# Kernel optimization log

Hardware: AMD Instinct MI355X
Metric: run time of the kernel (lower is better)

Reference implementation:

```python
import jax, jax.numpy as jnp
from jax import lax
import numpy as np

B, L, F = 4, 1024, 32
DM, NL, DS, DC, EX, NH = 256, 4, 16, 4, 2, 4
DI = EX * DM            # 512 inner channels
DTR = (DM + 15) // 16   # dt_rank = 16


def setup_inputs() -> dict:
    key = jax.random.key(0)
    ks = jax.random.split(key, 12)
    s = 0.02
    rn = lambda k, shape: jax.random.normal(k, shape, jnp.float32) * s
    return dict(
        x=jax.random.normal(ks[0], (B, L, F), jnp.float32),
        proj_w=rn(ks[1], (DM, F)), proj_b=jnp.zeros((DM,), jnp.float32),
        inproj_w=rn(ks[2], (NL, 2 * DI, DM)),
        conv_w=rn(ks[3], (NL, DI, DC)), conv_b=jnp.zeros((NL, DI), jnp.float32),
        xproj_w=rn(ks[4], (NL, DTR + 2 * DS, DI)),
        dtproj_w=rn(ks[5], (NL, DI, DTR)), dtproj_b=rn(ks[6], (NL, DI)),
        A_log=jnp.tile(jnp.log(jnp.arange(1, DS + 1, dtype=jnp.float32))[None, None, :], (NL, DI, 1)),
        Dp=jnp.ones((NL, DI), jnp.float32),
        outproj_w=rn(ks[7], (NL, DM, DI)),
        ln_g=jnp.ones((NL, DM), jnp.float32), ln_b=jnp.zeros((NL, DM), jnp.float32),
        head_w1=rn(ks[8], (DM, DM)), head_b1=jnp.zeros((DM,), jnp.float32),
        head_w2=rn(ks[9], (NH, DM)), head_b2=jnp.zeros((NH,), jnp.float32),
    )


def _layernorm(x, g, b, eps=1e-5):
    mu = x.mean(axis=-1, keepdims=True)
    var = ((x - mu) ** 2).mean(axis=-1, keepdims=True)
    return (x - mu) * lax.rsqrt(var + eps) * g + b


def _mamba(x, inw, cw, cb, xpw, dtw, dtb, A_log, Dp, outw):
    b, l, _ = x.shape
    xz = x @ inw.T                       # (b,l,2*DI)
    u, z = xz[..., :DI], xz[..., DI:]
    # causal depthwise conv1d, kernel DC
    up = jnp.pad(u, ((0, 0), (DC - 1, 0), (0, 0)))
    uc = sum(up[:, k:k + l, :] * cw[:, k] for k in range(DC)) + cb
    uc = jax.nn.silu(uc)
    dbc = uc @ xpw.T                     # (b,l,DTR+2*DS)
    dt, Bc, Cc = dbc[..., :DTR], dbc[..., DTR:DTR + DS], dbc[..., DTR + DS:]
    delta = jax.nn.softplus(dt @ dtw.T + dtb)   # (b,l,DI)
    A = -jnp.exp(A_log)                  # (DI,DS)

    def step(h, inp):
        d_t, B_t, C_t, u_t = inp         # (b,DI),(b,DS),(b,DS),(b,DI)
        h = jnp.exp(d_t[..., None] * A) * h + (d_t * u_t)[..., None] * B_t[:, None, :]
        return h, jnp.einsum('bdn,bn->bd', h, C_t)

    h0 = jnp.zeros((b, DI, DS), x.dtype)
    xs = tuple(jnp.swapaxes(a, 0, 1) for a in (delta, Bc, Cc, uc))
    _, ys = lax.scan(step, h0, xs)       # ys: (l,b,DI)
    y = jnp.swapaxes(ys, 0, 1) + uc * Dp
    return (y * jax.nn.silu(z)) @ outw.T


def reference(x, proj_w, proj_b, inproj_w, conv_w, conv_b, xproj_w, dtproj_w, dtproj_b,
              A_log, Dp, outproj_w, ln_g, ln_b, head_w1, head_b1, head_w2, head_b2):
    h = x @ proj_w.T + proj_b
    for i in range(NL):
        blk = _mamba(h, inproj_w[i], conv_w[i], conv_b[i], xproj_w[i],
                     dtproj_w[i], dtproj_b[i], A_log[i], Dp[i], outproj_w[i])
        h = h + _layernorm(blk, ln_g[i], ln_b[i])
    p = h.mean(axis=1)                   # (b,DM) pool over time
    hid = jax.nn.relu(p @ head_w1.T + head_b1)
    return hid @ head_w2.T + head_b2     # (b,NH)
```

## Files before the change

### kernel.cpp

```cpp
#include <hip/hip_runtime.h>
#include <hip/hip_fp16.h>
#include <math.h>

#define LTOT 1024
#define BB   4
#define F_IN 32
#define DM   256
#define DI   512
#define DS   16
#define DTRN 16
#define NXP  48
#define NLAY 4
#define NH   4
#define NC   16
#define CLEN 64
#define ROWS (BB*LTOT)

typedef _Float16 half8 __attribute__((ext_vector_type(8)));
typedef float f32x16 __attribute__((ext_vector_type(16)));

__device__ __forceinline__ float siluf_(float x) { return x / (1.0f + expf(-x)); }
__device__ __forceinline__ float softplusf_(float x) {
    if (x > 20.f) return x;
    if (x < -20.f) return expf(x);
    return log1pf(expf(x));
}

__device__ __forceinline__ void split16(float x, unsigned short& hi, unsigned short& lo) {
    __half h = __float2half(x);
    hi = *(unsigned short*)&h;
    float r = x - __half2float(h);
    __half l = __float2half(r);
    lo = *(unsigned short*)&l;
}

__global__ __launch_bounds__(256) void k_proj(const float* __restrict__ x,
                                              const float* __restrict__ pw,
                                              const float* __restrict__ pb,
                                              float* __restrict__ h) {
    __shared__ float wl[DM][33];
    __shared__ float xl[16][32];
    int t = threadIdx.x;
    int r0 = blockIdx.x * 16;
    for (int i = t; i < DM * 32 / 4; i += 256) {
        float4 v = ((const float4*)pw)[i];
        int c = i / 8, k = (i % 8) * 4;
        wl[c][k] = v.x; wl[c][k + 1] = v.y; wl[c][k + 2] = v.z; wl[c][k + 3] = v.w;
    }
    for (int i = t; i < 16 * 32 / 4; i += 256) {
        float4 v = ((const float4*)(x + (size_t)r0 * F_IN))[i];
        int r = i / 8, k = (i % 8) * 4;
        xl[r][k] = v.x; xl[r][k + 1] = v.y; xl[r][k + 2] = v.z; xl[r][k + 3] = v.w;
    }
    __syncthreads();
    int c = t;
    float bias = pb[c];
    float acc[16];
#pragma unroll
    for (int r = 0; r < 16; ++r) acc[r] = bias;
    for (int k = 0; k < 32; ++k) {
        float w = wl[c][k];
#pragma unroll
        for (int r = 0; r < 16; ++r) acc[r] = fmaf(xl[r][k], w, acc[r]);
    }
#pragma unroll
    for (int r = 0; r < 16; ++r) h[(size_t)(r0 + r) * DM + c] = acc[r];
}

__global__ __launch_bounds__(256) void k_gemm_xz(const float* __restrict__ A,
                                                 const float* __restrict__ Bw,
                                                 float* __restrict__ C) {
    __shared__ unsigned short Ah[128][40], Al[128][40], Bh[128][40], Bl[128][40];
    int t = threadIdx.x;
    int bx = blockIdx.x & 7;
    int by = blockIdx.x >> 3;
    int srow = t & 127, sh = t >> 7;
    const float* Ap = A + (size_t)(by * 128 + srow) * DM + sh * 16;
    const float* Bp = Bw + (size_t)(bx * 128 + srow) * DM + sh * 16;
    float4 pa[4], pb[4];
#pragma unroll
    for (int j = 0; j < 4; ++j) {
        pa[j] = *(const float4*)(Ap + j * 4);
        pb[j] = *(const float4*)(Bp + j * 4);
    }
    int lane = t & 63, wid = t >> 6;
    int fr = lane & 31, fg = lane >> 5;
    f32x16 acc[4] = {};
    for (int k0 = 0; k0 < DM; k0 += 32) {
        __syncthreads();
#pragma unroll
        for (int j = 0; j < 4; ++j) {
            ushort4 h4, l4;
            split16(pa[j].x, h4.x, l4.x); split16(pa[j].y, h4.y, l4.y);
            split16(pa[j].z, h4.z, l4.z); split16(pa[j].w, h4.w, l4.w);
            *(ushort4*)&Ah[srow][sh * 16 + j * 4] = h4;
            *(ushort4*)&Al[srow][sh * 16 + j * 4] = l4;
            split16(pb[j].x, h4.x, l4.x); split16(pb[j].y, h4.y, l4.y);
            split16(pb[j].z, h4.z, l4.z); split16(pb[j].w, h4.w, l4.w);
            *(ushort4*)&Bh[srow][sh * 16 + j * 4] = h4;
            *(ushort4*)&Bl[srow][sh * 16 + j * 4] = l4;
        }
        __syncthreads();
        if (k0 + 32 < DM) {
#pragma unroll
            for (int j = 0; j < 4; ++j) {
                pa[j] = *(const float4*)(Ap + k0 + 32 + j * 4);
                pb[j] = *(const float4*)(Bp + k0 + 32 + j * 4);
            }
        }
#pragma unroll
        for (int s = 0; s < 2; ++s) {
            int ko = s * 16 + fg * 8;
            half8 ah = *(const half8*)&Ah[wid * 32 + fr][ko];
            half8 al = *(const half8*)&Al[wid * 32 + fr][ko];
#pragma unroll
            for (int fc = 0; fc < 4; ++fc) {
                half8 bh = *(const half8*)&Bh[fc * 32 + fr][ko];
                half8 bl = *(const half8*)&Bl[fc * 32 + fr][ko];
                acc[fc] = __builtin_amdgcn_mfma_f32_32x32x16_f16(ah, bh, acc[fc], 0, 0, 0);
                acc[fc] = __builtin_amdgcn_mfma_f32_32x32x16_f16(ah, bl, acc[fc], 0, 0, 0);
                acc[fc] = __builtin_amdgcn_mfma_f32_32x32x16_f16(al, bh, acc[fc], 0, 0, 0);
            }
        }
    }
    float* Cp = C + (size_t)(by * 128 + wid * 32) * 1024 + bx * 128;
#pragma unroll
    for (int fc = 0; fc < 4; ++fc) {
#pragma unroll
        for (int reg = 0; reg < 16; ++reg) {
            int row = (reg & 3) + 8 * (reg >> 2) + 4 * fg;
            Cp[(size_t)row * 1024 + fc * 32 + fr] = acc[fc][reg];
        }
    }
}

__global__ __launch_bounds__(256) void k_conv(const float* __restrict__ xz,
                                              const float* __restrict__ cw,
                                              const float* __restrict__ cb,
                                              float* __restrict__ uc) {
    int gid = blockIdx.x * 256 + threadIdx.x;
    if (gid >= ROWS * (DI / 4)) return;
    int r = gid / (DI / 4);
    int d = (gid % (DI / 4)) * 4;
    int tt = r & (LTOT - 1);
    float4 acc = make_float4(cb[d], cb[d + 1], cb[d + 2], cb[d + 3]);
#pragma unroll
    for (int k = 0; k < 4; ++k) {
        int ts = tt - 3 + k;
        if (ts < 0) continue;
        float4 u = *(const float4*)(xz + (size_t)(r - 3 + k) * 1024 + d);
        acc.x = fmaf(u.x, cw[(d + 0) * 4 + k], acc.x);
        acc.y = fmaf(u.y, cw[(d + 1) * 4 + k], acc.y);
        acc.z = fmaf(u.z, cw[(d + 2) * 4 + k], acc.z);
        acc.w = fmaf(u.w, cw[(d + 3) * 4 + k], acc.w);
    }
    acc.x = siluf_(acc.x); acc.y = siluf_(acc.y); acc.z = siluf_(acc.z); acc.w = siluf_(acc.w);
    *(float4*)(uc + (size_t)r * DI + d) = acc;
}

__global__ __launch_bounds__(256) void k_dbcp(const float* __restrict__ uc,
                                              const float* __restrict__ xpw,
                                              float* __restrict__ xz) {
    __shared__ float us[32][132];
    __shared__ float wsd[48][132];
    int t = threadIdx.x;
    int kp = blockIdx.x & 3;
    int r0 = (blockIdx.x >> 2) * 32;
    int k0 = kp * 128;
    float4* us4 = (float4*)us;
    float4* ws4 = (float4*)wsd;
#pragma unroll
    for (int j = 0; j < 4; ++j) {
        int i = t + j * 256;
        int r = i >> 5, kq = i & 31;
        us4[r * 33 + kq] = *(const float4*)(uc + (size_t)(r0 + r) * DI + k0 + kq * 4);
    }
#pragma unroll
    for (int j = 0; j < 6; ++j) {
        int i = t + j * 256;
        int r = i >> 5, kq = i & 31;
        ws4[r * 33 + kq] = *(const float4*)(xpw + (size_t)r * DI + k0 + kq * 4);
    }
    __syncthreads();
    int tx = t & 15, ty = t >> 4;
    const float4* ua = us4 + (ty * 2) * 33;
    const float4* ub = ua + 33;
    const float4* w0p = ws4 + (tx * 3) * 33;
    const float4* w1p = w0p + 33;
    const float4* w2p = w0p + 66;
    float acc[2][3] = {};
#pragma unroll 4
    for (int kq = 0; kq < 32; ++kq) {
        float4 u0 = ua[kq], u1 = ub[kq];
        float4 w0 = w0p[kq], w1 = w1p[kq], w2 = w2p[kq];
        acc[0][0] = fmaf(u0.x, w0.x, acc[0][0]); acc[0][0] = fmaf(u0.y, w0.y, acc[0][0]);
        acc[0][0] = fmaf(u0.z, w0.z, acc[0][0]); acc[0][0] = fmaf(u0.w, w0.w, acc[0][0]);
        acc[0][1] = fmaf(u0.x, w1.x, acc[0][1]); acc[0][1] = fmaf(u0.y, w1.y, acc[0][1]);
        acc[0][1] = fmaf(u0.z, w1.z, acc[0][1]); acc[0][1] = fmaf(u0.w, w1.w, acc[0][1]);
        acc[0][2] = fmaf(u0.x, w2.x, acc[0][2]); acc[0][2] = fmaf(u0.y, w2.y, acc[0][2]);
        acc[0][2] = fmaf(u0.z, w2.z, acc[0][2]); acc[0][2] = fmaf(u0.w, w2.w, acc[0][2]);
        acc[1][0] = fmaf(u1.x, w0.x, acc[1][0]); acc[1][0] = fmaf(u1.y, w0.y, acc[1][0]);
        acc[1][0] = fmaf(u1.z, w0.z, acc[1][0]); acc[1][0] = fmaf(u1.w, w0.w, acc[1][0]);
        acc[1][1] = fmaf(u1.x, w1.x, acc[1][1]); acc[1][1] = fmaf(u1.y, w1.y, acc[1][1]);
        acc[1][1] = fmaf(u1.z, w1.z, acc[1][1]); acc[1][1] = fmaf(u1.w, w1.w, acc[1][1]);
        acc[1][2] = fmaf(u1.x, w2.x, acc[1][2]); acc[1][2] = fmaf(u1.y, w2.y, acc[1][2]);
        acc[1][2] = fmaf(u1.z, w2.z, acc[1][2]); acc[1][2] = fmaf(u1.w, w2.w, acc[1][2]);
    }
    float* outp = xz + (size_t)(r0 + ty * 2) * 1024 + kp * 48 + tx * 3;
    outp[0] = acc[0][0]; outp[1] = acc[0][1]; outp[2] = acc[0][2];
    outp[1024] = acc[1][0]; outp[1025] = acc[1][1]; outp[1026] = acc[1][2];
}

__global__ __launch_bounds__(256) void k_dbcr(const float* __restrict__ xzp,
                                              const float* __restrict__ dtw,
                                              const float* __restrict__ dtb,
                                              float* __restrict__ delta,
                                              float* __restrict__ BC) {
    __shared__ float dbl[16][NXP];
    int t = threadIdx.x;
    int r0 = blockIdx.x * 16;
    {
        int r = t >> 4, c3 = (t & 15) * 3;
        const float* pp = xzp + (size_t)(r0 + r) * 1024 + c3;
#pragma unroll
        for (int j = 0; j < 3; ++j) {
            float s = pp[j] + pp[48 + j] + pp[96 + j] + pp[144 + j];
            dbl[r][c3 + j] = s;
            int cj = c3 + j;
            if (cj >= 16) BC[(size_t)(r0 + r) * 32 + (cj - 16)] = s;
        }
    }
    __syncthreads();
    {
        int c0 = t * 2;
        float wd0[16], wd1[16];
        const float4* q0 = (const float4*)(dtw + (size_t)c0 * 16);
        const float4* q1 = (const float4*)(dtw + (size_t)(c0 + 1) * 16);
#pragma unroll
        for (int j = 0; j < 4; ++j) { *(float4*)&wd0[j * 4] = q0[j]; *(float4*)&wd1[j * 4] = q1[j]; }
        float bb0 = dtb[c0], bb1 = dtb[c0 + 1];
        for (int r = 0; r < 16; ++r) {
            float s0 = bb0, s1 = bb1;
#pragma unroll
            for (int k = 0; k < 16; ++k) {
                float dv = dbl[r][k];
                s0 = fmaf(dv, wd0[k], s0);
                s1 = fmaf(dv, wd1[k], s1);
            }
            *(float2*)(delta + (size_t)(r0 + r) * DI + c0) =
                make_float2(softplusf_(s0), softplusf_(s1));
        }
    }
}

__global__ __launch_bounds__(256) void k_scanA(const float* __restrict__ delta,
                                               const float* __restrict__ uc,
                                               const float* __restrict__ BC,
                                               const float* __restrict__ A_log,
                                               float* __restrict__ P,
                                               float* __restrict__ hL) {
    __shared__ float2 du2[CLEN][16];
    __shared__ float  Bl[CLEN][16];
    int bid = blockIdx.x;
    int c = bid & 15, dblk = (bid >> 4) & 31, b = bid >> 9;
    int d0 = dblk * 16, t0 = c * CLEN;
    int t = threadIdx.x;
    {
        int row = t >> 2, hf = (t & 3) * 4;
        size_t rbase = (size_t)(b * LTOT + t0 + row);
        float4 dv = *(const float4*)(delta + rbase * DI + d0 + hf);
        float4 uv = *(const float4*)(uc + rbase * DI + d0 + hf);
        float4* dst = (float4*)&du2[row][hf];
        dst[0] = make_float4(dv.x, uv.x, dv.y, uv.y);
        dst[1] = make_float4(dv.z, uv.z, dv.w, uv.w);
        *(float4*)&Bl[row][hf] = *(const float4*)(BC + rbase * 32 + hf);
    }
    __syncthreads();
    int n = t & 15, dn = t >> 4;
    float Ac = -expf(A_log[(size_t)(d0 + dn) * DS + n]);
    float h = 0.f, Pp = 1.f;
#pragma unroll 8
    for (int k = 0; k < CLEN; ++k) {
        float2 du = du2[k][dn];
        float Bv = Bl[k][n];
        float a = expf(du.x * Ac);
        Pp *= a;
        h = fmaf(a, h, du.x * du.y * Bv);
    }
    size_t idx = ((size_t)(b * NC + c)) * (DI * DS) + (size_t)d0 * DS + t;
    P[idx] = Pp;
    hL[idx] = h;
}

__global__ __launch_bounds__(256) void k_scanC(const float* __restrict__ delta,
                                               const float* __restrict__ uc,
                                               const float* __restrict__ BC,
                                               const float* __restrict__ A_log,
                                               const float* __restrict__ P,
                                               const float* __restrict__ hL,
                                               const float* __restrict__ Dp,
                                               float* __restrict__ xz) {
    __shared__ float2 du2[CLEN][16];
    __shared__ float2 bc2[CLEN][16];
    __shared__ float  ytmp[16][16][20];
    int bid = blockIdx.x;
    int c = bid & 15, dblk = (bid >> 4) & 31, b = bid >> 9;
    int d0 = dblk * 16, t0 = c * CLEN;
    int t = threadIdx.x;
    {
        int row = t >> 2, hf = (t & 3) * 4;
        size_t rbase = (size_t)(b * LTOT + t0 + row);
        float4 dv = *(const float4*)(delta + rbase * DI + d0 + hf);
        float4 uv = *(const float4*)(uc + rbase * DI + d0 + hf);
        float4* dst = (float4*)&du2[row][hf];
        dst[0] = make_float4(dv.x, uv.x, dv.y, uv.y);
        dst[1] = make_float4(dv.z, uv.z, dv.w, uv.w);
        float4 bv = *(const float4*)(BC + rbase * 32 + hf);
        float4 cv = *(const float4*)(BC + rbase * 32 + 16 + hf);
        float4* bdst = (float4*)&bc2[row][hf];
        bdst[0] = make_float4(bv.x, cv.x, bv.y, cv.y);
        bdst[1] = make_float4(bv.z, cv.z, bv.w, cv.w);
    }
    __syncthreads();
    int n = t & 15, dn = t >> 4;
    float Ac = -expf(A_log[(size_t)(d0 + dn) * DS + n]);
    float Hin = 0.f;
    for (int cc = 0; cc < c; ++cc) {
        size_t idx = ((size_t)(b * NC + cc)) * (DI * DS) + (size_t)d0 * DS + t;
        Hin = fmaf(P[idx], Hin, hL[idx]);
    }
    float h = Hin;
    int rdn = t & 15, rk = t >> 4;
    float DpV = Dp[d0 + rdn];
    for (int s = 0; s < CLEN / 16; ++s) {
#pragma unroll
        for (int kk = 0; kk < 16; ++kk) {
            int k = s * 16 + kk;
            float2 du = du2[k][dn];
            float2 bc = bc2[k][n];
            float a = expf(du.x * Ac);
            h = fmaf(a, h, du.x * du.y * bc.x);
            ytmp[kk][dn][n] = h * bc.y;
        }
        __syncthreads();
        {
            const float* rowp = &ytmp[rk][rdn][0];
            float4 v0 = *(const float4*)(rowp + 0);
            float4 v1 = *(const float4*)(rowp + 4);
            float4 v2 = *(const float4*)(rowp + 8);
            float4 v3 = *(const float4*)(rowp + 12);
            float y = ((v0.x + v0.y) + (v0.z + v0.w)) + ((v1.x + v1.y) + (v1.z + v1.w))
                    + ((v2.x + v2.y) + (v2.z + v2.w)) + ((v3.x + v3.y) + (v3.z + v3.w));
            float uu = du2[s * 16 + rk][rdn].y;
            size_t rb2 = (size_t)(b * LTOT + t0 + s * 16 + rk);
            float z = xz[rb2 * 1024 + 512 + d0 + rdn];
            xz[rb2 * 1024 + d0 + rdn] = fmaf(uu, DpV, y) * siluf_(z);
        }
        __syncthreads();
    }
}

__global__ __launch_bounds__(256) void k_gemm_out(const float* __restrict__ xz,
                                                  const float* __restrict__ outw,
                                                  float* __restrict__ p01,
                                                  float* __restrict__ p23) {
    __shared__ unsigned short Ah[128][40], Al[128][40], Bh[128][40], Bl[128][40];
    int t = threadIdx.x;
    int bx = blockIdx.x & 1;
    int by = (blockIdx.x >> 1) & 31;
    int kp = blockIdx.x >> 6;
    int srow = t & 127, sh = t >> 7;
    const float* Ap = xz + (size_t)(by * 128 + srow) * 1024 + kp * 128 + sh * 16;
    const float* Bp = outw + (size_t)(bx * 128 + srow) * DI + kp * 128 + sh * 16;
    float4 pa[4], pb[4];
#pragma unroll
    for (int j = 0; j < 4; ++j) {
        pa[j] = *(const float4*)(Ap + j * 4);
        pb[j] = *(const float4*)(Bp + j * 4);
    }
    int lane = t & 63, wid = t >> 6;
    int fr = lane & 31, fg = lane >> 5;
    f32x16 acc[4] = {};
    for (int k0 = 0; k0 < 128; k0 += 32) {
        __syncthreads();
#pragma unroll
        for (int j = 0; j < 4; ++j) {
            ushort4 h4, l4;
            split16(pa[j].x, h4.x, l4.x); split16(pa[j].y, h4.y, l4.y);
            split16(pa[j].z, h4.z, l4.z); split16(pa[j].w, h4.w, l4.w);
            *(ushort4*)&Ah[srow][sh * 16 + j * 4] = h4;
            *(ushort4*)&Al[srow][sh * 16 + j * 4] = l4;
            split16(pb[j].x, h4.x, l4.x); split16(pb[j].y, h4.y, l4.y);
            split16(pb[j].z, h4.z, l4.z); split16(pb[j].w, h4.w, l4.w);
            *(ushort4*)&Bh[srow][sh * 16 + j * 4] = h4;
            *(ushort4*)&Bl[srow][sh * 16 + j * 4] = l4;
        }
        __syncthreads();
        if (k0 + 32 < 128) {
#pragma unroll
            for (int j = 0; j < 4; ++j) {
                pa[j] = *(const float4*)(Ap + k0 + 32 + j * 4);
                pb[j] = *(const float4*)(Bp + k0 + 32 + j * 4);
            }
        }
#pragma unroll
        for (int s = 0; s < 2; ++s) {
            int ko = s * 16 + fg * 8;
            half8 ah = *(const half8*)&Ah[wid * 32 + fr][ko];
            half8 al = *(const half8*)&Al[wid * 32 + fr][ko];
#pragma unroll
            for (int fc = 0; fc < 4; ++fc) {
                half8 bh = *(const half8*)&Bh[fc * 32 + fr][ko];
                half8 bl = *(const half8*)&Bl[fc * 32 + fr][ko];
                acc[fc] = __builtin_amdgcn_mfma_f32_32x32x16_f16(ah, bh, acc[fc], 0, 0, 0);
                acc[fc] = __builtin_amdgcn_mfma_f32_32x32x16_f16(ah, bl, acc[fc], 0, 0, 0);
                acc[fc] = __builtin_amdgcn_mfma_f32_32x32x16_f16(al, bh, acc[fc], 0, 0, 0);
            }
        }
    }
    float* pbase = (kp < 2 ? p01 : p23) + (size_t)(kp & 1) * (ROWS * DM);
    float* Cp = pbase + (size_t)(by * 128 + wid * 32) * DM + bx * 128;
#pragma unroll
    for (int fc = 0; fc < 4; ++fc) {
#pragma unroll
        for (int reg = 0; reg < 16; ++reg) {
            int row = (reg & 3) + 8 * (reg >> 2) + 4 * fg;
            Cp[(size_t)row * DM + fc * 32 + fr] = acc[fc][reg];
        }
    }
}

__global__ __launch_bounds__(256) void k_ln_res(const float* __restrict__ p01,
                                                const float* __restrict__ p23,
                                                const float* __restrict__ g,
                                                const float* __restrict__ bb,
                                                float* __restrict__ h) {
    __shared__ float scratch[4];
    int r = blockIdx.x, t = threadIdx.x;
    size_t idx = (size_t)r * DM + t;
    float v = p01[idx] + p01[idx + (size_t)ROWS * DM] + p23[idx] + p23[idx + (size_t)ROWS * DM];
    float s = v;
#pragma unroll
    for (int m = 32; m >= 1; m >>= 1) s += __shfl_xor(s, m, 64);
    if ((t & 63) == 0) scratch[t >> 6] = s;
    __syncthreads();
    float mu = (scratch[0] + scratch[1] + scratch[2] + scratch[3]) * (1.f / DM);
    __syncthreads();
    float d = v - mu;
    float s2 = d * d;
#pragma unroll
    for (int m = 32; m >= 1; m >>= 1) s2 += __shfl_xor(s2, m, 64);
    if ((t & 63) == 0) scratch[t >> 6] = s2;
    __syncthreads();
    float var = (scratch[0] + scratch[1] + scratch[2] + scratch[3]) * (1.f / DM);
    float rstd = 1.f / sqrtf(var + 1e-5f);
    h[idx] += d * rstd * g[t] + bb[t];
}

__global__ __launch_bounds__(256) void k_meanp(const float* __restrict__ h,
                                               float* __restrict__ part) {
    int bid = blockIdx.x;
    int b = bid >> 3, g = bid & 7;
    int t = threadIdx.x;
    float s = 0.f;
    for (int k = 0; k < 128; ++k)
        s += h[(size_t)(b * LTOT + g * 128 + k) * DM + t];
    part[(size_t)bid * DM + t] = s;
}

__global__ __launch_bounds__(256) void k_head(const float* __restrict__ part,
                                              const float* __restrict__ w1,
                                              const float* __restrict__ b1,
                                              const float* __restrict__ w2,
                                              const float* __restrict__ b2,
                                              float* __restrict__ out) {
    __shared__ float pl[DM], hl[DM];
    int b = blockIdx.x, t = threadIdx.x;
    float s = 0.f;
    for (int g = 0; g < 8; ++g) s += part[(size_t)(b * 8 + g) * DM + t];
    pl[t] = s * (1.f / LTOT);
    __syncthreads();
    float a = b1[t];
    for (int k = 0; k < DM; ++k) a = fmaf(pl[k], w1[(size_t)t * DM + k], a);
    hl[t] = fmaxf(a, 0.f);
    __syncthreads();
    if (t < NH) {
        float o = b2[t];
        for (int k = 0; k < DM; ++k) o = fmaf(hl[k], w2[(size_t)t * DM + k], o);
        out[b * NH + t] = o;
    }
}

extern "C" void kernel_launch(void* const* d_in, const int* in_sizes, int n_in,
                              void* d_out, int out_size, void* d_ws, size_t ws_size,
                              hipStream_t stream) {
    const float* x        = (const float*)d_in[0];
    const float* proj_w   = (const float*)d_in[1];
    const float* proj_b   = (const float*)d_in[2];
    const float* inproj_w = (const float*)d_in[3];
    const float* conv_w   = (const float*)d_in[4];
    const float* conv_b   = (const float*)d_in[5];
    const float* xproj_w  = (const float*)d_in[6];
    const float* dtproj_w = (const float*)d_in[7];
    const float* dtproj_b = (const float*)d_in[8];
    const float* A_log    = (const float*)d_in[9];
    const float* Dp       = (const float*)d_in[10];
    const float* outproj_w= (const float*)d_in[11];
    const float* ln_g     = (const float*)d_in[12];
    const float* ln_b     = (const float*)d_in[13];
    const float* head_w1  = (const float*)d_in[14];
    const float* head_b1  = (const float*)d_in[15];
    const float* head_w2  = (const float*)d_in[16];
    const float* head_b2  = (const float*)d_in[17];

    float* ws    = (float*)d_ws;
    float* h     = ws;
    float* xz    = h + 1048576;
    float* uc    = xz + 4194304;
    float* delta = uc + 2097152;
    float* BC    = delta + 2097152;
    float* Pbuf  = BC + 131072;
    float* hLbuf = Pbuf + 524288;
    float* part  = hLbuf + 524288;

    k_proj<<<ROWS / 16, 256, 0, stream>>>(x, proj_w, proj_b, h);

    for (int i = 0; i < NLAY; ++i) {
        const float* inw  = inproj_w + (size_t)i * (2 * DI) * DM;
        const float* cwi  = conv_w + (size_t)i * DI * 4;
        const float* cbi  = conv_b + (size_t)i * DI;
        const float* xpw  = xproj_w + (size_t)i * NXP * DI;
        const float* dtw  = dtproj_w + (size_t)i * DI * DTRN;
        const float* dtb  = dtproj_b + (size_t)i * DI;
        const float* Ali  = A_log + (size_t)i * DI * DS;
        const float* Dpi  = Dp + (size_t)i * DI;
        const float* outw = outproj_w + (size_t)i * DM * DI;
        const float* gi   = ln_g + (size_t)i * DM;
        const float* bi   = ln_b + (size_t)i * DM;

        k_gemm_xz<<<256, 256, 0, stream>>>(h, inw, xz);
        k_conv<<<ROWS * (DI / 4) / 256, 256, 0, stream>>>(xz, cwi, cbi, uc);
        k_dbcp<<<512, 256, 0, stream>>>(uc, xpw, xz);
        k_dbcr<<<ROWS / 16, 256, 0, stream>>>(xz, dtw, dtb, delta, BC);
        k_scanA<<<BB * 32 * NC, 256, 0, stream>>>(delta, uc, BC, Ali, Pbuf, hLbuf);
        k_scanC<<<BB * 32 * NC, 256, 0, stream>>>(delta, uc, BC, Ali, Pbuf, hLbuf, Dpi, xz);
        k_gemm_out<<<256, 256, 0, stream>>>(xz, outw, delta, uc);
        k_ln_res<<<ROWS, 256, 0, stream>>>(delta, uc, gi, bi, h);
    }

    k_meanp<<<32, 256, 0, stream>>>(h, part);
    k_head<<<BB, 256, 0, stream>>>(part, head_w1, head_b1, head_w2, head_b2, (float*)d_out);
}
```

Baseline: 533.5 us.

## Pre-split GEMM operands into fp16 hi/lo in producers and shrink GEMM tiles

Weights for in_proj and out_proj are split into fp16 hi/lo halves once per call by a new kernel. Activations are split in the producing kernels (proj, layernorm-residual, scanC) and written as separate hi/lo buffers, so the GEMMs load ready-made halves instead of converting inside the main loop. The GEMM tile shrinks from 128x128 to 64x128, doubling the grid to 512 blocks for better occupancy. The cost is extra global writes for the hi/lo buffers, more workspace, and one added kernel launch.

```diff
diff --git a/kernel.cpp b/kernel.cpp
--- a/kernel.cpp
+++ b/kernel.cpp
@@ -18,6 +18,7 @@
 
 typedef _Float16 half8 __attribute__((ext_vector_type(8)));
 typedef float f32x16 __attribute__((ext_vector_type(16)));
+typedef unsigned short us8 __attribute__((ext_vector_type(8)));
 
 __device__ __forceinline__ float siluf_(float x) { return x / (1.0f + expf(-x)); }
 __device__ __forceinline__ float softplusf_(float x) {
@@ -34,10 +35,36 @@
     lo = *(unsigned short*)&l;
 }
 
+__global__ __launch_bounds__(256) void k_splitw(const float* __restrict__ inw,
+                                                const float* __restrict__ outw,
+                                                unsigned short* __restrict__ iwh,
+                                                unsigned short* __restrict__ iwl,
+                                                unsigned short* __restrict__ owh,
+                                                unsigned short* __restrict__ owl) {
+    int q = blockIdx.x * 256 + threadIdx.x;
+    ushort4 h4, l4;
+    if (q < 262144) {
+        float4 v = ((const float4*)inw)[q];
+        split16(v.x, h4.x, l4.x); split16(v.y, h4.y, l4.y);
+        split16(v.z, h4.z, l4.z); split16(v.w, h4.w, l4.w);
+        *(ushort4*)(iwh + (size_t)q * 4) = h4;
+        *(ushort4*)(iwl + (size_t)q * 4) = l4;
+    } else {
+        int r = q - 262144;
+        float4 v = ((const float4*)outw)[r];
+        split16(v.x, h4.x, l4.x); split16(v.y, h4.y, l4.y);
+        split16(v.z, h4.z, l4.z); split16(v.w, h4.w, l4.w);
+        *(ushort4*)(owh + (size_t)r * 4) = h4;
+        *(ushort4*)(owl + (size_t)r * 4) = l4;
+    }
+}
+
 __global__ __launch_bounds__(256) void k_proj(const float* __restrict__ x,
                                               const float* __restrict__ pw,
                                               const float* __restrict__ pb,
-                                              float* __restrict__ h) {
+                                              float* __restrict__ h,
+                                              unsigned short* __restrict__ hh,
+                                              unsigned short* __restrict__ hl) {
     __shared__ float wl[DM][33];
     __shared__ float xl[16][32];
     int t = threadIdx.x;
@@ -64,68 +91,66 @@
         for (int r = 0; r < 16; ++r) acc[r] = fmaf(xl[r][k], w, acc[r]);
     }
 #pragma unroll
-    for (int r = 0; r < 16; ++r) h[(size_t)(r0 + r) * DM + c] = acc[r];
-}
-
-__global__ __launch_bounds__(256) void k_gemm_xz(const float* __restrict__ A,
-                                                 const float* __restrict__ Bw,
+    for (int r = 0; r < 16; ++r) {
+        size_t idx = (size_t)(r0 + r) * DM + c;
+        h[idx] = acc[r];
+        unsigned short vh, vl; split16(acc[r], vh, vl);
+        hh[idx] = vh; hl[idx] = vl;
+    }
+}
+
+__global__ __launch_bounds__(256) void k_gemm_xz(const unsigned short* __restrict__ Ahp,
+                                                 const unsigned short* __restrict__ Alp,
+                                                 const unsigned short* __restrict__ Bhp,
+                                                 const unsigned short* __restrict__ Blp,
                                                  float* __restrict__ C) {
-    __shared__ unsigned short Ah[128][40], Al[128][40], Bh[128][40], Bl[128][40];
+    __shared__ unsigned short Ah[64][40], Al[64][40], Bh[128][40], Bl[128][40];
     int t = threadIdx.x;
     int bx = blockIdx.x & 7;
     int by = blockIdx.x >> 3;
-    int srow = t & 127, sh = t >> 7;
-    const float* Ap = A + (size_t)(by * 128 + srow) * DM + sh * 16;
-    const float* Bp = Bw + (size_t)(bx * 128 + srow) * DM + sh * 16;
-    float4 pa[4], pb[4];
-#pragma unroll
-    for (int j = 0; j < 4; ++j) {
-        pa[j] = *(const float4*)(Ap + j * 4);
-        pb[j] = *(const float4*)(Bp + j * 4);
-    }
+    int rowA = t >> 2, kA = (t & 3) * 8;
+    int rowB = t >> 1, kB = (t & 1) * 16;
+    const unsigned short* ApH = Ahp + (size_t)(by * 64 + rowA) * DM + kA;
+    const unsigned short* ApL = Alp + (size_t)(by * 64 + rowA) * DM + kA;
+    const unsigned short* BpH = Bhp + (size_t)(bx * 128 + rowB) * DM + kB;
+    const unsigned short* BpL = Blp + (size_t)(bx * 128 + rowB) * DM + kB;
+    us8 rah = *(const us8*)ApH, ral = *(const us8*)ApL;
+    us8 rbh0 = *(const us8*)BpH, rbh1 = *(const us8*)(BpH + 8);
+    us8 rbl0 = *(const us8*)BpL, rbl1 = *(const us8*)(BpL + 8);
     int lane = t & 63, wid = t >> 6;
     int fr = lane & 31, fg = lane >> 5;
-    f32x16 acc[4] = {};
+    int wr = wid >> 1, wc = wid & 1;
+    f32x16 acc[2] = {};
     for (int k0 = 0; k0 < DM; k0 += 32) {
-        __syncthreads();
-#pragma unroll
-        for (int j = 0; j < 4; ++j) {
-            ushort4 h4, l4;
-            split16(pa[j].x, h4.x, l4.x); split16(pa[j].y, h4.y, l4.y);
-            split16(pa[j].z, h4.z, l4.z); split16(pa[j].w, h4.w, l4.w);
-            *(ushort4*)&Ah[srow][sh * 16 + j * 4] = h4;
-            *(ushort4*)&Al[srow][sh * 16 + j * 4] = l4;
-            split16(pb[j].x, h4.x, l4.x); split16(pb[j].y, h4.y, l4.y);
-            split16(pb[j].z, h4.z, l4.z); split16(pb[j].w, h4.w, l4.w);
-            *(ushort4*)&Bh[srow][sh * 16 + j * 4] = h4;
-            *(ushort4*)&Bl[srow][sh * 16 + j * 4] = l4;
-        }
+        *(us8*)&Ah[rowA][kA] = rah;
+        *(us8*)&Al[rowA][kA] = ral;
+        *(us8*)&Bh[rowB][kB] = rbh0; *(us8*)&Bh[rowB][kB + 8] = rbh1;
+        *(us8*)&Bl[rowB][kB] = rbl0; *(us8*)&Bl[rowB][kB + 8] = rbl1;
         __syncthreads();
         if (k0 + 32 < DM) {
-#pragma unroll
-            for (int j = 0; j < 4; ++j) {
-                pa[j] = *(const float4*)(Ap + k0 + 32 + j * 4);
-                pb[j] = *(const float4*)(Bp + k0 + 32 + j * 4);
-            }
+            rah = *(const us8*)(ApH + k0 + 32); ral = *(const us8*)(ApL + k0 + 32);
+            rbh0 = *(const us8*)(BpH + k0 + 32); rbh1 = *(const us8*)(BpH + k0 + 40);
+            rbl0 = *(const us8*)(BpL + k0 + 32); rbl1 = *(const us8*)(BpL + k0 + 40);
         }
 #pragma unroll
         for (int s = 0; s < 2; ++s) {
             int ko = s * 16 + fg * 8;
-            half8 ah = *(const half8*)&Ah[wid * 32 + fr][ko];
-            half8 al = *(const half8*)&Al[wid * 32 + fr][ko];
-#pragma unroll
-            for (int fc = 0; fc < 4; ++fc) {
-                half8 bh = *(const half8*)&Bh[fc * 32 + fr][ko];
-                half8 bl = *(const half8*)&Bl[fc * 32 + fr][ko];
+            half8 ah = *(const half8*)&Ah[wr * 32 + fr][ko];
+            half8 al = *(const half8*)&Al[wr * 32 + fr][ko];
+#pragma unroll
+            for (int fc = 0; fc < 2; ++fc) {
+                half8 bh = *(const half8*)&Bh[wc * 64 + fc * 32 + fr][ko];
+                half8 bl = *(const half8*)&Bl[wc * 64 + fc * 32 + fr][ko];
                 acc[fc] = __builtin_amdgcn_mfma_f32_32x32x16_f16(ah, bh, acc[fc], 0, 0, 0);
                 acc[fc] = __builtin_amdgcn_mfma_f32_32x32x16_f16(ah, bl, acc[fc], 0, 0, 0);
                 acc[fc] = __builtin_amdgcn_mfma_f32_32x32x16_f16(al, bh, acc[fc], 0, 0, 0);
             }
         }
-    }
-    float* Cp = C + (size_t)(by * 128 + wid * 32) * 1024 + bx * 128;
-#pragma unroll
-    for (int fc = 0; fc < 4; ++fc) {
+        __syncthreads();
+    }
+    float* Cp = C + (size_t)(by * 64 + wr * 32) * 1024 + bx * 128 + wc * 64;
+#pragma unroll
+    for (int fc = 0; fc < 2; ++fc) {
 #pragma unroll
         for (int reg = 0; reg < 16; ++reg) {
             int row = (reg & 3) + 8 * (reg >> 2) + 4 * fg;
@@ -299,7 +324,9 @@
                                                const float* __restrict__ P,
                                                const float* __restrict__ hL,
                                                const float* __restrict__ Dp,
-                                               float* __restrict__ xz) {
+                                               const float* __restrict__ xz,
+                                               unsigned short* __restrict__ yh,
+                                               unsigned short* __restrict__ yl) {
     __shared__ float2 du2[CLEN][16];
     __shared__ float2 bc2[CLEN][16];
     __shared__ float  ytmp[16][16][20];
@@ -354,74 +381,70 @@
             float uu = du2[s * 16 + rk][rdn].y;
             size_t rb2 = (size_t)(b * LTOT + t0 + s * 16 + rk);
             float z = xz[rb2 * 1024 + 512 + d0 + rdn];
-            xz[rb2 * 1024 + d0 + rdn] = fmaf(uu, DpV, y) * siluf_(z);
+            float val = fmaf(uu, DpV, y) * siluf_(z);
+            unsigned short vh, vl; split16(val, vh, vl);
+            size_t yi = rb2 * DI + d0 + rdn;
+            yh[yi] = vh; yl[yi] = vl;
         }
         __syncthreads();
     }
 }
 
-__global__ __launch_bounds__(256) void k_gemm_out(const float* __restrict__ xz,
-                                                  const float* __restrict__ outw,
+__global__ __launch_bounds__(256) void k_gemm_out(const unsigned short* __restrict__ Ahp,
+                                                  const unsigned short* __restrict__ Alp,
+                                                  const unsigned short* __restrict__ Bhp,
+                                                  const unsigned short* __restrict__ Blp,
                                                   float* __restrict__ p01,
                                                   float* __restrict__ p23) {
-    __shared__ unsigned short Ah[128][40], Al[128][40], Bh[128][40], Bl[128][40];
+    __shared__ unsigned short Ah[64][40], Al[64][40], Bh[128][40], Bl[128][40];
     int t = threadIdx.x;
     int bx = blockIdx.x & 1;
-    int by = (blockIdx.x >> 1) & 31;
-    int kp = blockIdx.x >> 6;
-    int srow = t & 127, sh = t >> 7;
-    const float* Ap = xz + (size_t)(by * 128 + srow) * 1024 + kp * 128 + sh * 16;
-    const float* Bp = outw + (size_t)(bx * 128 + srow) * DI + kp * 128 + sh * 16;
-    float4 pa[4], pb[4];
-#pragma unroll
-    for (int j = 0; j < 4; ++j) {
-        pa[j] = *(const float4*)(Ap + j * 4);
-        pb[j] = *(const float4*)(Bp + j * 4);
-    }
+    int by = (blockIdx.x >> 1) & 63;
+    int kp = blockIdx.x >> 7;
+    int rowA = t >> 2, kA = (t & 3) * 8;
+    int rowB = t >> 1, kB = (t & 1) * 16;
+    const unsigned short* ApH = Ahp + (size_t)(by * 64 + rowA) * DI + kp * 128 + kA;
+    const unsigned short* ApL = Alp + (size_t)(by * 64 + rowA) * DI + kp * 128 + kA;
+    const unsigned short* BpH = Bhp + (size_t)(bx * 128 + rowB) * DI + kp * 128 + kB;
+    const unsigned short* BpL = Blp + (size_t)(bx * 128 + rowB) * DI + kp * 128 + kB;
+    us8 rah = *(const us8*)ApH, ral = *(const us8*)ApL;
+    us8 rbh0 = *(const us8*)BpH, rbh1 = *(const us8*)(BpH + 8);
+    us8 rbl0 = *(const us8*)BpL, rbl1 = *(const us8*)(BpL + 8);
     int lane = t & 63, wid = t >> 6;
     int fr = lane & 31, fg = lane >> 5;
-    f32x16 acc[4] = {};
+    int wr = wid >> 1, wc = wid & 1;
+    f32x16 acc[2] = {};
     for (int k0 = 0; k0 < 128; k0 += 32) {
-        __syncthreads();
-#pragma unroll
-        for (int j = 0; j < 4; ++j) {
-            ushort4 h4, l4;
-            split16(pa[j].x, h4.x, l4.x); split16(pa[j].y, h4.y, l4.y);
-            split16(pa[j].z, h4.z, l4.z); split16(pa[j].w, h4.w, l4.w);
-            *(ushort4*)&Ah[srow][sh * 16 + j * 4] = h4;
-            *(ushort4*)&Al[srow][sh * 16 + j * 4] = l4;
-            split16(pb[j].x, h4.x, l4.x); split16(pb[j].y, h4.y, l4.y);
-            split16(pb[j].z, h4.z, l4.z); split16(pb[j].w, h4.w, l4.w);
-            *(ushort4*)&Bh[srow][sh * 16 + j * 4] = h4;
-            *(ushort4*)&Bl[srow][sh * 16 + j * 4] = l4;
-        }
+        *(us8*)&Ah[rowA][kA] = rah;
+        *(us8*)&Al[rowA][kA] = ral;
+        *(us8*)&Bh[rowB][kB] = rbh0; *(us8*)&Bh[rowB][kB + 8] = rbh1;
+        *(us8*)&Bl[rowB][kB] = rbl0; *(us8*)&Bl[rowB][kB + 8] = rbl1;
         __syncthreads();
         if (k0 + 32 < 128) {
-#pragma unroll
-            for (int j = 0; j < 4; ++j) {
-                pa[j] = *(const float4*)(Ap + k0 + 32 + j * 4);
-                pb[j] = *(const float4*)(Bp + k0 + 32 + j * 4);
-            }
+            rah = *(const us8*)(ApH + k0 + 32); ral = *(const us8*)(ApL + k0 + 32);
+            rbh0 = *(const us8*)(BpH + k0 + 32); rbh1 = *(const us8*)(BpH + k0 + 40);
+            rbl0 = *(const us8*)(BpL + k0 + 32); rbl1 = *(const us8*)(BpL + k0 + 40);
         }
 #pragma unroll
         for (int s = 0; s < 2; ++s) {
             int ko = s * 16 + fg * 8;
-            half8 ah = *(const half8*)&Ah[wid * 32 + fr][ko];
-            half8 al = *(const half8*)&Al[wid * 32 + fr][ko];
-#pragma unroll
-            for (int fc = 0; fc < 4; ++fc) {
-                half8 bh = *(const half8*)&Bh[fc * 32 + fr][ko];
-                half8 bl = *(const half8*)&Bl[fc * 32 + fr][ko];
+            half8 ah = *(const half8*)&Ah[wr * 32 + fr][ko];
+            half8 al = *(const half8*)&Al[wr * 32 + fr][ko];
+#pragma unroll
+            for (int fc = 0; fc < 2; ++fc) {
+                half8 bh = *(const half8*)&Bh[wc * 64 + fc * 32 + fr][ko];
+                half8 bl = *(const half8*)&Bl[wc * 64 + fc * 32 + fr][ko];
                 acc[fc] = __builtin_amdgcn_mfma_f32_32x32x16_f16(ah, bh, acc[fc], 0, 0, 0);
                 acc[fc] = __builtin_amdgcn_mfma_f32_32x32x16_f16(ah, bl, acc[fc], 0, 0, 0);
                 acc[fc] = __builtin_amdgcn_mfma_f32_32x32x16_f16(al, bh, acc[fc], 0, 0, 0);
             }
         }
+        __syncthreads();
     }
     float* pbase = (kp < 2 ? p01 : p23) + (size_t)(kp & 1) * (ROWS * DM);
-    float* Cp = pbase + (size_t)(by * 128 + wid * 32) * DM + bx * 128;
-#pragma unroll
-    for (int fc = 0; fc < 4; ++fc) {
+    float* Cp = pbase + (size_t)(by * 64 + wr * 32) * DM + bx * 128 + wc * 64;
+#pragma unroll
+    for (int fc = 0; fc < 2; ++fc) {
 #pragma unroll
         for (int reg = 0; reg < 16; ++reg) {
             int row = (reg & 3) + 8 * (reg >> 2) + 4 * fg;
@@ -434,7 +457,9 @@
                                                 const float* __restrict__ p23,
                                                 const float* __restrict__ g,
                                                 const float* __restrict__ bb,
-                                                float* __restrict__ h) {
+                                                float* __restrict__ h,
+                                                unsigned short* __restrict__ hh,
+                                                unsigned short* __restrict__ hl) {
     __shared__ float scratch[4];
     int r = blockIdx.x, t = threadIdx.x;
     size_t idx = (size_t)r * DM + t;
@@ -454,7 +479,10 @@
     __syncthreads();
     float var = (scratch[0] + scratch[1] + scratch[2] + scratch[3]) * (1.f / DM);
     float rstd = 1.f / sqrtf(var + 1e-5f);
-    h[idx] += d * rstd * g[t] + bb[t];
+    float nv = h[idx] + d * rstd * g[t] + bb[t];
+    h[idx] = nv;
+    unsigned short vh, vl; split16(nv, vh, vl);
+    hh[idx] = vh; hl[idx] = vl;
 }
 
 __global__ __launch_bounds__(256) void k_meanp(const float* __restrict__ h,
@@ -522,11 +550,19 @@
     float* Pbuf  = BC + 131072;
     float* hLbuf = Pbuf + 524288;
     float* part  = hLbuf + 524288;
-
-    k_proj<<<ROWS / 16, 256, 0, stream>>>(x, proj_w, proj_b, h);
+    unsigned short* h_hi  = (unsigned short*)(part + 8192);
+    unsigned short* h_lo  = h_hi + 1048576;
+    unsigned short* y_hi  = h_lo + 1048576;
+    unsigned short* y_lo  = y_hi + 2097152;
+    unsigned short* iw_hi = y_lo + 2097152;
+    unsigned short* iw_lo = iw_hi + 1048576;
+    unsigned short* ow_hi = iw_lo + 1048576;
+    unsigned short* ow_lo = ow_hi + 524288;
+
+    k_splitw<<<1536, 256, 0, stream>>>(inproj_w, outproj_w, iw_hi, iw_lo, ow_hi, ow_lo);
+    k_proj<<<ROWS / 16, 256, 0, stream>>>(x, proj_w, proj_b, h, h_hi, h_lo);
 
     for (int i = 0; i < NLAY; ++i) {
-        const float* inw  = inproj_w + (size_t)i * (2 * DI) * DM;
         const float* cwi  = conv_w + (size_t)i * DI * 4;
         const float* cbi  = conv_b + (size_t)i * DI;
         const float* xpw  = xproj_w + (size_t)i * NXP * DI;
@@ -534,18 +570,20 @@
         const float* dtb  = dtproj_b + (size_t)i * DI;
         const float* Ali  = A_log + (size_t)i * DI * DS;
         const float* Dpi  = Dp + (size_t)i * DI;
-        const float* outw = outproj_w + (size_t)i * DM * DI;
         const float* gi   = ln_g + (size_t)i * DM;
         const float* bi   = ln_b + (size_t)i * DM;
 
-        k_gemm_xz<<<256, 256, 0, stream>>>(h, inw, xz);
+        k_gemm_xz<<<512, 256, 0, stream>>>(h_hi, h_lo,
+                                           iw_hi + (size_t)i * 262144, iw_lo + (size_t)i * 262144, xz);
         k_conv<<<ROWS * (DI / 4) / 256, 256, 0, stream>>>(xz, cwi, cbi, uc);
         k_dbcp<<<512, 256, 0, stream>>>(uc, xpw, xz);
         k_dbcr<<<ROWS / 16, 256, 0, stream>>>(xz, dtw, dtb, delta, BC);
         k_scanA<<<BB * 32 * NC, 256, 0, stream>>>(delta, uc, BC, Ali, Pbuf, hLbuf);
-        k_scanC<<<BB * 32 * NC, 256, 0, stream>>>(delta, uc, BC, Ali, Pbuf, hLbuf, Dpi, xz);
-        k_gemm_out<<<256, 256, 0, stream>>>(xz, outw, delta, uc);
-        k_ln_res<<<ROWS, 256, 0, stream>>>(delta, uc, gi, bi, h);
+        k_scanC<<<BB * 32 * NC, 256, 0, stream>>>(delta, uc, BC, Ali, Pbuf, hLbuf, Dpi, xz, y_hi, y_lo);
+        k_gemm_out<<<512, 256, 0, stream>>>(y_hi, y_lo,
+                                            ow_hi + (size_t)i * 131072, ow_lo + (size_t)i * 131072,
+                                            delta, uc);
+        k_ln_res<<<ROWS, 256, 0, stream>>>(delta, uc, gi, bi, h, h_hi, h_lo);
     }
 
     k_meanp<<<32, 256, 0, stream>>>(h, part);
```

Measured after the change: 507.0 us. 1.05x faster.
